# Kernel tuning notes

Hardware: AMD Instinct MI355X
Metric: run time of the kernel (lower is better)

The kernel has to match this reference:

```python
import jax, jax.numpy as jnp
import numpy as np

B, S, DIM = 2, 2048, 2048
NH = 16
Q_LORA, KV_LORA = 1536, 512
NOPE, ROPE, VHD = 128, 64, 128
QK_HD = NOPE + ROPE  # 192
EPS = 1e-6
SCALE = QK_HD ** -0.5


def rmsnorm(x, w, eps=EPS):
    return x * jax.lax.rsqrt(jnp.mean(x * x, axis=-1, keepdims=True) + eps) * w


def apply_rope(x, cos, sin):
    # x: (b, s, h, d) with d even; cos/sin: (s, d//2)
    xr, xi = x[..., 0::2], x[..., 1::2]
    c = cos[None, :, None, :]
    s = sin[None, :, None, :]
    yr = xr * c - xi * s
    yi = xr * s + xi * c
    return jnp.stack([yr, yi], axis=-1).reshape(x.shape)


def setup_inputs() -> dict:
    key = jax.random.key(0)
    ks = jax.random.split(key, 12)
    std = 0.02
    # RoPE tables (unit-magnitude complex as cos/sin)
    inv_freq = 1.0 / (10000.0 ** (np.arange(0, ROPE, 2, dtype=np.float32) / ROPE))  # (32,)
    ang = np.arange(S, dtype=np.float32)[:, None] * inv_freq[None, :]  # (S, 32)
    return {
        "x": jax.random.normal(ks[0], (B, S, DIM), jnp.float32),
        "freqs_cos": jnp.asarray(np.cos(ang)),
        "freqs_sin": jnp.asarray(np.sin(ang)),
        "wq_a_w": jax.random.normal(ks[1], (Q_LORA, DIM), jnp.float32) * std,
        "wq_a_b": jnp.zeros((Q_LORA,), jnp.float32),
        "q_norm_w": jnp.ones((Q_LORA,), jnp.float32),
        "wq_b_w": jax.random.normal(ks[2], (NH * QK_HD, Q_LORA), jnp.float32) * std,
        "wq_b_b": jnp.zeros((NH * QK_HD,), jnp.float32),
        "wkv_a_w": jax.random.normal(ks[3], (KV_LORA + ROPE, DIM), jnp.float32) * std,
        "wkv_a_b": jnp.zeros((KV_LORA + ROPE,), jnp.float32),
        "kv_norm_w": jnp.ones((KV_LORA,), jnp.float32),
        "wkv_b_w": jax.random.normal(ks[4], (NH * (NOPE + VHD), KV_LORA), jnp.float32) * std,
        "wkv_b_b": jnp.zeros((NH * (NOPE + VHD),), jnp.float32),
        "wo_w": jax.random.normal(ks[5], (DIM, NH * VHD), jnp.float32) * std,
        "wo_b": jnp.zeros((DIM,), jnp.float32),
    }


def reference(x, freqs_cos, freqs_sin, wq_a_w, wq_a_b, q_norm_w, wq_b_w, wq_b_b,
              wkv_a_w, wkv_a_b, kv_norm_w, wkv_b_w, wkv_b_b, wo_w, wo_b):
    b, s, _ = x.shape
    # Low-rank Q projection: wq_b(q_norm(wq_a(x)))
    q = rmsnorm(x @ wq_a_w.T + wq_a_b, q_norm_w) @ wq_b_w.T + wq_b_b
    q = q.reshape(b, s, NH, QK_HD)
    q_nope, q_pe = q[..., :NOPE], q[..., NOPE:]
    q = jnp.concatenate([q_nope, apply_rope(q_pe, freqs_cos, freqs_sin)], axis=-1)
    # Low-rank KV projection
    kv = x @ wkv_a_w.T + wkv_a_b  # (b, s, kv_lora + rope)
    kv_c, k_pe = kv[..., :KV_LORA], kv[..., KV_LORA:]
    k_pe = apply_rope(k_pe[:, :, None, :], freqs_cos, freqs_sin)  # (b, s, 1, rope)
    kv = rmsnorm(kv_c, kv_norm_w) @ wkv_b_w.T + wkv_b_b
    kv = kv.reshape(b, s, NH, NOPE + VHD)
    k_nope, v = kv[..., :NOPE], kv[..., NOPE:]
    k = jnp.concatenate([k_nope, jnp.broadcast_to(k_pe, (b, s, NH, ROPE))], axis=-1)
    # Causal SDPA
    scores = jnp.einsum("bqhd,bkhd->bhqk", q, k) * SCALE
    causal = jnp.tril(jnp.ones((s, s), bool))
    scores = jnp.where(causal[None, None], scores, jnp.float32(-1e30))
    attn = jax.nn.softmax(scores, axis=-1)
    out = jnp.einsum("bhqk,bkhd->bqhd", attn, v).reshape(b, s, NH * VHD)
    return out @ wo_w.T + wo_b
```

## Files before the change

kernel.cpp:

```cpp
#include <hip/hip_runtime.h>


typedef __bf16 bf16x8 __attribute__((ext_vector_type(8)));
typedef float f32x4 __attribute__((ext_vector_type(4)));
typedef unsigned short u16;

#define SEQ 2048
#define SCALE 0.07216878364870323f
#define NEGBIG -30000.0f

__device__ __forceinline__ float b2f(u16 u) {
  union { unsigned u; float f; } c; c.u = ((unsigned)u) << 16; return c.f;
}
__device__ __forceinline__ u16 f2b(float f) {
  union { float f; unsigned u; } c; c.f = f;
  unsigned r = (c.u + 0x7fffu + ((c.u >> 16) & 1u)) >> 16;
  return (u16)r;
}
__device__ __forceinline__ uint4 pack8(float4 a, float4 b) {
  union { uint4 v; u16 e[8]; } t;
  t.e[0] = f2b(a.x); t.e[1] = f2b(a.y); t.e[2] = f2b(a.z); t.e[3] = f2b(a.w);
  t.e[4] = f2b(b.x); t.e[5] = f2b(b.y); t.e[6] = f2b(b.z); t.e[7] = f2b(b.w);
  return t.v;
}

#define GLOAD_LDS16(gsrc, ldst)                                              \
  __builtin_amdgcn_global_load_lds(                                          \
      (const __attribute__((address_space(1))) unsigned int*)(gsrc),         \
      (__attribute__((address_space(3))) unsigned int*)(ldst), 16, 0, 0)

__global__ void cvt_kernel(const float* __restrict__ src, u16* __restrict__ dst,
                           long n8) {
  long i = (long)blockIdx.x * 256 + threadIdx.x;
  long stride = (long)gridDim.x * 256;
  for (; i < n8; i += stride) {
    const float4* s = (const float4*)(src + i * 8);
    float4 a = s[0], b = s[1];
    *(uint4*)(dst + i * 8) = pack8(a, b);
  }
}

template <int OF>
__global__ __launch_bounds__(256) void gemm_lds_kernel(
    const u16* __restrict__ X, int lda, const u16* __restrict__ W,
    const float* __restrict__ bias, void* __restrict__ out,
    int N, int K, float oscale) {
  __shared__ alignas(16) u16 As[2][128 * 64];
  __shared__ alignas(16) u16 Bs[2][128 * 64];
  const int tid = threadIdx.x;
  const int wave = tid >> 6, lane = tid & 63;
  const int quad = lane >> 4, l16 = lane & 15;
  const int wr = (wave >> 1) * 64, wc = (wave & 1) * 64;
  const int bm = blockIdx.x * 128, bn = blockIdx.y * 128;
  const int srow0 = wave * 32 + (lane >> 3);
  const int gcol = ((lane & 7) ^ (lane >> 3)) * 8;

  f32x4 acc[4][4] = {};

  auto stage = [&](int buf, int k0) {
#pragma unroll
    for (int p = 0; p < 4; ++p) {
      int row = srow0 + p * 8;
      const u16* ga = X + (size_t)(bm + row) * lda + k0 + gcol;
      const u16* gb = W + (size_t)(bn + row) * K + k0 + gcol;
      char* la = (char*)(&As[buf][0]) + (wave * 4 + p) * 1024;
      char* lb = (char*)(&Bs[buf][0]) + (wave * 4 + p) * 1024;
      GLOAD_LDS16(ga, la);
      GLOAD_LDS16(gb, lb);
    }
  };

  const int nk = K >> 6;
  stage(0, 0);
  int cur = 0;
  for (int kt = 0; kt < nk; ++kt) {
    __syncthreads();
    if (kt + 1 < nk) stage(cur ^ 1, (kt + 1) * 64);
    const u16* as = &As[cur][0];
    const u16* bs = &Bs[cur][0];
#pragma unroll
    for (int kk = 0; kk < 64; kk += 32) {
      const int cs = (kk + quad * 8) ^ ((l16 & 7) * 8);
      bf16x8 a[4], b[4];
#pragma unroll
      for (int i = 0; i < 4; ++i)
        a[i] = *(const bf16x8*)(as + (wr + i * 16 + l16) * 64 + cs);
#pragma unroll
      for (int j = 0; j < 4; ++j)
        b[j] = *(const bf16x8*)(bs + (wc + j * 16 + l16) * 64 + cs);
#pragma unroll
      for (int i = 0; i < 4; ++i)
#pragma unroll
        for (int j = 0; j < 4; ++j)
          acc[i][j] = __builtin_amdgcn_mfma_f32_16x16x32_bf16(a[i], b[j], acc[i][j], 0, 0, 0);
    }
    cur ^= 1;
  }

#pragma unroll
  for (int i = 0; i < 4; ++i)
#pragma unroll
    for (int j = 0; j < 4; ++j) {
      int col = bn + wc + j * 16 + l16;
      float bv = bias[col];
#pragma unroll
      for (int r = 0; r < 4; ++r) {
        int row = bm + wr + i * 16 + quad * 4 + r;
        float v = (acc[i][j][r] + bv) * oscale;
        if (OF) ((float*)out)[(size_t)row * N + col] = v;
        else    ((u16*)out)[(size_t)row * N + col] = f2b(v);
      }
    }
}

template <int XF, int WF, int OF>
__global__ __launch_bounds__(256, 3) void gemm_kernel(
    const void* __restrict__ X, int lda, const void* __restrict__ W,
    const float* __restrict__ bias, void* __restrict__ out,
    int M, int N, int K, float oscale) {
  constexpr int LDT = 72;
  __shared__ alignas(16) u16 As[64 * LDT];
  __shared__ alignas(16) u16 Bs[128 * LDT];
  const int tid = threadIdx.x;
  const int wave = tid >> 6, lane = tid & 63;
  const int quad = lane >> 4, l16 = lane & 15;
  const int bm = blockIdx.x * 64, bn = blockIdx.y * 128;
  const int wn = wave * 32;
  const int srow = tid >> 3;
  const int scol = (tid & 7) * 8;

  f32x4 acc[4][2] = {};

  float4 pa32[2][2], pb32[4][2];
  uint4  pa16[2],    pb16[4];

  auto load_tile = [&](int k0) {
#pragma unroll
    for (int p = 0; p < 2; ++p) {
      size_t off = (size_t)(bm + srow + p * 32) * lda + k0 + scol;
      if (XF) {
        const float* s = (const float*)X + off;
        pa32[p][0] = *(const float4*)s;
        pa32[p][1] = *(const float4*)(s + 4);
      } else {
        pa16[p] = *(const uint4*)((const u16*)X + off);
      }
    }
#pragma unroll
    for (int p = 0; p < 4; ++p) {
      int n = bn + srow + p * 32;
      size_t off = (size_t)n * K + k0 + scol;
      if (WF) {
        if (n < N) {
          const float* s = (const float*)W + off;
          pb32[p][0] = *(const float4*)s;
          pb32[p][1] = *(const float4*)(s + 4);
        } else {
          pb32[p][0] = make_float4(0.f, 0.f, 0.f, 0.f);
          pb32[p][1] = make_float4(0.f, 0.f, 0.f, 0.f);
        }
      } else {
        if (n < N) pb16[p] = *(const uint4*)((const u16*)W + off);
        else { pb16[p].x = pb16[p].y = pb16[p].z = pb16[p].w = 0u; }
      }
    }
  };

  load_tile(0);
  for (int k0 = 0; k0 < K; k0 += 64) {
    __syncthreads();
#pragma unroll
    for (int p = 0; p < 2; ++p) {
      uint4 v;
      if (XF) v = pack8(pa32[p][0], pa32[p][1]); else v = pa16[p];
      *(uint4*)(&As[(srow + p * 32) * LDT + scol]) = v;
    }
#pragma unroll
    for (int p = 0; p < 4; ++p) {
      uint4 v;
      if (WF) v = pack8(pb32[p][0], pb32[p][1]); else v = pb16[p];
      *(uint4*)(&Bs[(srow + p * 32) * LDT + scol]) = v;
    }
    __syncthreads();
    if (k0 + 64 < K) load_tile(k0 + 64);

#pragma unroll
    for (int kk = 0; kk < 64; kk += 32) {
      bf16x8 a[4], b[2];
#pragma unroll
      for (int i = 0; i < 4; ++i)
        a[i] = *(const bf16x8*)(&As[(i * 16 + l16) * LDT + kk + quad * 8]);
#pragma unroll
      for (int j = 0; j < 2; ++j)
        b[j] = *(const bf16x8*)(&Bs[(wn + j * 16 + l16) * LDT + kk + quad * 8]);
#pragma unroll
      for (int i = 0; i < 4; ++i)
#pragma unroll
        for (int j = 0; j < 2; ++j)
          acc[i][j] = __builtin_amdgcn_mfma_f32_16x16x32_bf16(a[i], b[j], acc[i][j], 0, 0, 0);
    }
  }

#pragma unroll
  for (int i = 0; i < 4; ++i)
#pragma unroll
    for (int j = 0; j < 2; ++j) {
      int col = bn + wn + j * 16 + l16;
      if (col < N) {
        float bv = bias[col];
#pragma unroll
        for (int r = 0; r < 4; ++r) {
          int row = bm + i * 16 + quad * 4 + r;
          float v = (acc[i][j][r] + bv) * oscale;
          if (OF) ((float*)out)[(size_t)row * N + col] = v;
          else    ((u16*)out)[(size_t)row * N + col] = f2b(v);
        }
      }
    }
}

__global__ void rmsnorm_kernel(u16* x, const float* __restrict__ w,
                               int C, int stride) {
  size_t base = (size_t)blockIdx.x * stride;
  float s = 0.f;
  for (int c = threadIdx.x; c < C; c += 256) { float v = b2f(x[base + c]); s += v * v; }
#pragma unroll
  for (int off = 32; off > 0; off >>= 1) s += __shfl_xor(s, off, 64);
  __shared__ float red[4];
  if ((threadIdx.x & 63) == 0) red[threadIdx.x >> 6] = s;
  __syncthreads();
  float tot = red[0] + red[1] + red[2] + red[3];
  float scale = rsqrtf(tot / (float)C + 1e-6f);
  for (int c = threadIdx.x; c < C; c += 256)
    x[base + c] = f2b(b2f(x[base + c]) * scale * w[c]);
}

__global__ void rope_kpe_kernel(const u16* __restrict__ kvn,
                                const float* __restrict__ fcos,
                                const float* __restrict__ fsin,
                                u16* __restrict__ kpe) {
  int idx = blockIdx.x * 256 + threadIdx.x;
  int t = idx >> 5, i = idx & 31;
  int s = t & (SEQ - 1);
  float c = fcos[s * 32 + i], sn = fsin[s * 32 + i];
  float xr = b2f(kvn[(size_t)t * 576 + 512 + 2 * i]);
  float xi = b2f(kvn[(size_t)t * 576 + 512 + 2 * i + 1]);
  kpe[(size_t)t * 64 + 2 * i]     = f2b(xr * c - xi * sn);
  kpe[(size_t)t * 64 + 2 * i + 1] = f2b(xr * sn + xi * c);
}

__global__ void rope_q_kernel(u16* q, const float* __restrict__ fcos,
                              const float* __restrict__ fsin) {
  int idx = blockIdx.x * 256 + threadIdx.x;
  int t = idx >> 8, h = (idx >> 5) & 7, i = idx & 31;
  int s = t & (SEQ - 1);
  float c = fcos[s * 32 + i], sn = fsin[s * 32 + i];
  size_t base = (size_t)t * 1536 + h * 192 + 128 + 2 * i;
  float xr = b2f(q[base]), xi = b2f(q[base + 1]);
  q[base]     = f2b(xr * c - xi * sn);
  q[base + 1] = f2b(xr * sn + xi * c);
}

template <int PAIRED>
__global__ __launch_bounds__(256, 2) void attn_kernel(
    const u16* __restrict__ Q0,
    const u16* __restrict__ Q1,
    const u16* __restrict__ KV0,
    const u16* __restrict__ KV1,
    const u16* __restrict__ KPE,
    u16* __restrict__ O,
    int hbase) {
  constexpr int LK = 200;
  constexpr int LP = 72;
  __shared__ alignas(16) u16 Ks[64 * LK];
  __shared__ alignas(16) u16 Ps[64 * LP];
  __shared__ alignas(16) u16 Vs[128 * LP];

  const int tid = threadIdx.x;
  const int wave = tid >> 6, lane = tid & 63;
  const int quad = lane >> 4, l16 = lane & 15;
  const int h = hbase + blockIdx.y;
  const int hl = h & 7;
  const u16* __restrict__ Q   = (h & 8) ? Q1  : Q0;
  const u16* __restrict__ KVB = (h & 8) ? KV1 : KV0;
  const size_t tok0 = (size_t)blockIdx.z * SEQ;

  auto process = [&](int qt) {
    const int q0 = qt * 64;
    bf16x8 qf[6];
    {
      const u16* qp = Q + (tok0 + q0 + wave * 16 + l16) * 1536 + hl * 192 + quad * 8;
#pragma unroll
      for (int c = 0; c < 6; ++c) qf[c] = *(const bf16x8*)(qp + c * 32);
    }

    f32x4 o_acc[8] = {};
    float m_i[4], l_i[4];
#pragma unroll
    for (int r = 0; r < 4; ++r) { m_i[r] = NEGBIG; l_i[r] = 0.f; }

    const int nkt = qt + 1;
    uint4 kreg[6], vreg[4];
    auto load_tile = [&](int kt) {
      int k0 = kt * 64;
#pragma unroll
      for (int p = 0; p < 6; ++p) {
        int flat = tid + p * 256;
        int r = flat / 24, c8 = (flat % 24) * 8;
        const u16* src = (c8 < 128)
            ? (KVB + (tok0 + k0 + r) * 2048 + hl * 256 + c8)
            : (KPE + (tok0 + k0 + r) * 64 + (c8 - 128));
        kreg[p] = *(const uint4*)src;
      }
#pragma unroll
      for (int p = 0; p < 4; ++p) {
        int flat = tid + p * 256;
        int r = flat / 16, c8 = (flat % 16) * 8;
        vreg[p] = *(const uint4*)(KVB + (tok0 + k0 + r) * 2048 + hl * 256 + 128 + c8);
      }
    };

    load_tile(0);
    for (int kt = 0; kt < nkt; ++kt) {
      const int k0 = kt * 64;
      __syncthreads();
#pragma unroll
      for (int p = 0; p < 6; ++p) {
        int flat = tid + p * 256;
        int r = flat / 24, c8 = (flat % 24) * 8;
        *(uint4*)(&Ks[r * LK + c8]) = kreg[p];
      }
#pragma unroll
      for (int p = 0; p < 4; ++p) {
        int flat = tid + p * 256;
        int r = flat / 16, c8 = (flat % 16) * 8;
        union { uint4 v4; u16 e[8]; } t;
        t.v4 = vreg[p];
        int rs = r >> 3, rl = r & 7;
#pragma unroll
        for (int j = 0; j < 8; ++j) {
          int n = c8 + j;
          Vs[n * LP + ((rs ^ ((n >> 3) & 7)) << 3) + rl] = t.e[j];
        }
      }
      __syncthreads();
      if (kt + 1 < nkt) load_tile(kt + 1);

      f32x4 sc[4];
#pragma unroll
      for (int ni = 0; ni < 4; ++ni) {
        f32x4 a = {};
#pragma unroll
        for (int c = 0; c < 6; ++c) {
          bf16x8 kf = *(const bf16x8*)(&Ks[(ni * 16 + l16) * LK + c * 32 + quad * 8]);
          a = __builtin_amdgcn_mfma_f32_16x16x32_bf16(qf[c], kf, a, 0, 0, 0);
        }
        sc[ni] = a;
      }

      const int qrow_base = q0 + wave * 16 + quad * 4;
      if (kt == nkt - 1) {
#pragma unroll
        for (int ni = 0; ni < 4; ++ni) {
          int col = k0 + ni * 16 + l16;
#pragma unroll
          for (int r = 0; r < 4; ++r)
            if (col > qrow_base + r) sc[ni][r] = NEGBIG;
        }
      }

      float mloc[4];
#pragma unroll
      for (int r = 0; r < 4; ++r) mloc[r] = NEGBIG;
#pragma unroll
      for (int ni = 0; ni < 4; ++ni)
#pragma unroll
        for (int r = 0; r < 4; ++r) mloc[r] = fmaxf(mloc[r], sc[ni][r]);
#pragma unroll
      for (int off = 1; off < 16; off <<= 1)
#pragma unroll
        for (int r = 0; r < 4; ++r) mloc[r] = fmaxf(mloc[r], __shfl_xor(mloc[r], off, 64));

      float alpha[4], rsum[4];
#pragma unroll
      for (int r = 0; r < 4; ++r) {
        float mn = fmaxf(m_i[r], mloc[r]);
        alpha[r] = __expf(m_i[r] - mn);
        m_i[r] = mn;
        rsum[r] = 0.f;
      }
#pragma unroll
      for (int ni = 0; ni < 4; ++ni)
#pragma unroll
        for (int r = 0; r < 4; ++r) {
          float p = __expf(sc[ni][r] - m_i[r]);
          sc[ni][r] = p;
          rsum[r] += p;
        }
#pragma unroll
      for (int off = 1; off < 16; off <<= 1)
#pragma unroll
        for (int r = 0; r < 4; ++r) rsum[r] += __shfl_xor(rsum[r], off, 64);
#pragma unroll
      for (int r = 0; r < 4; ++r) l_i[r] = l_i[r] * alpha[r] + rsum[r];

#pragma unroll
      for (int ni = 0; ni < 4; ++ni)
#pragma unroll
        for (int r = 0; r < 4; ++r)
          Ps[(wave * 16 + quad * 4 + r) * LP + ni * 16 + l16] = f2b(sc[ni][r]);

      __syncthreads();

#pragma unroll
      for (int t8 = 0; t8 < 8; ++t8)
#pragma unroll
        for (int r = 0; r < 4; ++r) o_acc[t8][r] *= alpha[r];

      bf16x8 pf0 = *(const bf16x8*)(&Ps[(wave * 16 + l16) * LP + quad * 8]);
      bf16x8 pf1 = *(const bf16x8*)(&Ps[(wave * 16 + l16) * LP + 32 + quad * 8]);
#pragma unroll
      for (int ni = 0; ni < 8; ++ni) {
        int n0 = ni * 16 + l16;
        int sw = (n0 >> 3) & 7;
        bf16x8 vf0 = *(const bf16x8*)(&Vs[n0 * LP + ((quad ^ sw) << 3)]);
        bf16x8 vf1 = *(const bf16x8*)(&Vs[n0 * LP + (((4 + quad) ^ sw) << 3)]);
        o_acc[ni] = __builtin_amdgcn_mfma_f32_16x16x32_bf16(pf0, vf0, o_acc[ni], 0, 0, 0);
        o_acc[ni] = __builtin_amdgcn_mfma_f32_16x16x32_bf16(pf1, vf1, o_acc[ni], 0, 0, 0);
      }
    }

#pragma unroll
    for (int ni = 0; ni < 8; ++ni) {
      int col = h * 128 + ni * 16 + l16;
#pragma unroll
      for (int r = 0; r < 4; ++r) {
        size_t row = tok0 + q0 + wave * 16 + quad * 4 + r;
        O[row * 2048 + col] = f2b(o_acc[ni][r] / l_i[r]);
      }
    }
  };

  if (PAIRED) {
    process(31 - (int)blockIdx.x);
    process((int)blockIdx.x);
  } else {
    process(blockIdx.z == 0 ? (31 - (int)blockIdx.x) : (int)blockIdx.x);
  }
}

extern "C" void kernel_launch(void* const* d_in, const int* in_sizes, int n_in,
                              void* d_out, int out_size, void* d_ws, size_t ws_size,
                              hipStream_t stream) {
  const float* x      = (const float*)d_in[0];
  const float* fcos   = (const float*)d_in[1];
  const float* fsin   = (const float*)d_in[2];
  const float* wqa    = (const float*)d_in[3];
  const float* wqa_b  = (const float*)d_in[4];
  const float* qnw    = (const float*)d_in[5];
  const float* wqb    = (const float*)d_in[6];
  const float* wqb_b  = (const float*)d_in[7];
  const float* wkva   = (const float*)d_in[8];
  const float* wkva_b = (const float*)d_in[9];
  const float* kvnw   = (const float*)d_in[10];
  const float* wkvb   = (const float*)d_in[11];
  const float* wkvb_b = (const float*)d_in[12];
  const float* wo     = (const float*)d_in[13];
  const float* wo_b   = (const float*)d_in[14];

  char* ws = (char*)d_ws;
  u16* qn   = (u16*)(ws + 0);
  u16* kvn  = (u16*)(ws + 12582912);
  u16* kpe  = (u16*)(ws + 17301504);
  u16* qbA  = (u16*)(ws + 17825792);
  u16* kvB  = (u16*)(ws + 30408704);
  u16* ao   = (u16*)(ws + 47185920);

  dim3 blk(256);

  if (ws_size >= 123994112u) {
    u16* xb    = (u16*)(ws + 63963136);
    u16* kvA   = (u16*)(ws + 63963136);
    u16* wqab  = (u16*)(ws + 80740352);
    u16* wkvab = (u16*)(ws + 87031808);
    u16* wqbb  = (u16*)(ws + 89391104);
    u16* wkvbw = (u16*)(ws + 98828288);
    u16* wob   = (u16*)(ws + 103022592);
    u16* qbB   = (u16*)(ws + 111411200);

    cvt_kernel<<<2048, blk, 0, stream>>>(x,    xb,    1048576);
    cvt_kernel<<<1536, blk, 0, stream>>>(wqa,  wqab,   393216);
    cvt_kernel<<< 576, blk, 0, stream>>>(wkva, wkvab,  147456);
    cvt_kernel<<<2048, blk, 0, stream>>>(wqb,  wqbb,   589824);
    cvt_kernel<<<1024, blk, 0, stream>>>(wkvb, wkvbw,  262144);
    cvt_kernel<<<2048, blk, 0, stream>>>(wo,   wob,    524288);

    gemm_lds_kernel<0><<<dim3(32, 12), blk, 0, stream>>>(xb, 2048, wqab, wqa_b, qn, 1536, 2048, 1.0f);
    gemm_kernel<0,0,0><<<dim3(64, 5),  blk, 0, stream>>>(xb, 2048, wkvab, wkva_b, kvn, 4096, 576, 2048, 1.0f);
    rmsnorm_kernel<<<4096, blk, 0, stream>>>(qn, qnw, 1536, 1536);
    rmsnorm_kernel<<<4096, blk, 0, stream>>>(kvn, kvnw, 512, 576);
    rope_kpe_kernel<<<512, blk, 0, stream>>>(kvn, fcos, fsin, kpe);

    gemm_lds_kernel<0><<<dim3(32, 12), blk, 0, stream>>>(qn, 1536, wqbb, wqb_b, qbA, 1536, 1536, SCALE);
    gemm_lds_kernel<0><<<dim3(32, 12), blk, 0, stream>>>(qn, 1536, wqbb + (size_t)1536 * 1536, wqb_b + 1536, qbB, 1536, 1536, SCALE);
    rope_q_kernel<<<4096, blk, 0, stream>>>(qbA, fcos, fsin);
    rope_q_kernel<<<4096, blk, 0, stream>>>(qbB, fcos, fsin);
    gemm_lds_kernel<0><<<dim3(32, 16), blk, 0, stream>>>(kvn, 576, wkvbw, wkvb_b, kvA, 2048, 512, 1.0f);
    gemm_lds_kernel<0><<<dim3(32, 16), blk, 0, stream>>>(kvn, 576, wkvbw + (size_t)2048 * 512, wkvb_b + 2048, kvB, 2048, 512, 1.0f);

    attn_kernel<1><<<dim3(16, 16, 2), blk, 0, stream>>>(qbA, qbB, kvA, kvB, kpe, ao, 0);

    gemm_lds_kernel<1><<<dim3(32, 16), blk, 0, stream>>>(ao, 2048, wob, wo_b, (float*)d_out, 2048, 2048, 1.0f);
  } else if (ws_size >= 111411200u) {
    u16* xb    = (u16*)(ws + 63963136);
    u16* wqab  = (u16*)(ws + 80740352);
    u16* wkvab = (u16*)(ws + 87031808);
    u16* wqbb  = (u16*)(ws + 89391104);
    u16* wkvbw = (u16*)(ws + 98828288);
    u16* wob   = (u16*)(ws + 103022592);

    cvt_kernel<<<2048, blk, 0, stream>>>(x,    xb,    1048576);
    cvt_kernel<<<1536, blk, 0, stream>>>(wqa,  wqab,   393216);
    cvt_kernel<<< 576, blk, 0, stream>>>(wkva, wkvab,  147456);
    cvt_kernel<<<2048, blk, 0, stream>>>(wqb,  wqbb,   589824);
    cvt_kernel<<<1024, blk, 0, stream>>>(wkvb, wkvbw,  262144);
    cvt_kernel<<<2048, blk, 0, stream>>>(wo,   wob,    524288);

    gemm_kernel<0,0,0><<<dim3(64, 12), blk, 0, stream>>>(xb, 2048, wqab, wqa_b, qn, 4096, 1536, 2048, 1.0f);
    gemm_kernel<0,0,0><<<dim3(64, 5),  blk, 0, stream>>>(xb, 2048, wkvab, wkva_b, kvn, 4096, 576, 2048, 1.0f);
    rmsnorm_kernel<<<4096, blk, 0, stream>>>(qn, qnw, 1536, 1536);
    rmsnorm_kernel<<<4096, blk, 0, stream>>>(kvn, kvnw, 512, 576);
    rope_kpe_kernel<<<512, blk, 0, stream>>>(kvn, fcos, fsin, kpe);

    for (int g = 0; g < 2; ++g) {
      const u16* wqb_g   = wqbb + (size_t)g * 1536 * 1536;
      const float* wqb_bg  = wqb_b + g * 1536;
      const u16* wkvb_g  = wkvbw + (size_t)g * 2048 * 512;
      const float* wkvb_bg = wkvb_b + g * 2048;
      gemm_kernel<0,0,0><<<dim3(64, 12), blk, 0, stream>>>(qn, 1536, wqb_g, wqb_bg, qbA, 4096, 1536, 1536, SCALE);
      rope_q_kernel<<<4096, blk, 0, stream>>>(qbA, fcos, fsin);
      gemm_kernel<0,0,0><<<dim3(64, 16), blk, 0, stream>>>(kvn, 576, wkvb_g, wkvb_bg, kvB, 4096, 2048, 512, 1.0f);
      attn_kernel<0><<<dim3(32, 8, 2), blk, 0, stream>>>(qbA, qbA, kvB, kvB, kpe, ao, g * 8);
    }

    gemm_kernel<0,0,1><<<dim3(64, 16), blk, 0, stream>>>(ao, 2048, wob, wo_b, (float*)d_out, 4096, 2048, 2048, 1.0f);
  } else {
    gemm_kernel<1,1,0><<<dim3(64, 12), blk, 0, stream>>>(x, 2048, wqa, wqa_b, qn, 4096, 1536, 2048, 1.0f);
    gemm_kernel<1,1,0><<<dim3(64, 5),  blk, 0, stream>>>(x, 2048, wkva, wkva_b, kvn, 4096, 576, 2048, 1.0f);
    rmsnorm_kernel<<<4096, blk, 0, stream>>>(qn, qnw, 1536, 1536);
    rmsnorm_kernel<<<4096, blk, 0, stream>>>(kvn, kvnw, 512, 576);
    rope_kpe_kernel<<<512, blk, 0, stream>>>(kvn, fcos, fsin, kpe);

    for (int g = 0; g < 2; ++g) {
      const float* wqb_g   = wqb + (size_t)g * 1536 * 1536;
      const float* wqb_bg  = wqb_b + g * 1536;
      const float* wkvb_g  = wkvb + (size_t)g * 2048 * 512;
      const float* wkvb_bg = wkvb_b + g * 2048;
      gemm_kernel<0,1,0><<<dim3(64, 12), blk, 0, stream>>>(qn, 1536, wqb_g, wqb_bg, qbA, 4096, 1536, 1536, SCALE);
      rope_q_kernel<<<4096, blk, 0, stream>>>(qbA, fcos, fsin);
      gemm_kernel<0,1,0><<<dim3(64, 16), blk, 0, stream>>>(kvn, 576, wkvb_g, wkvb_bg, kvB, 4096, 2048, 512, 1.0f);
      attn_kernel<0><<<dim3(32, 8, 2), blk, 0, stream>>>(qbA, qbA, kvB, kvB, kpe, ao, g * 8);
    }

    gemm_kernel<0,1,1><<<dim3(64, 16), blk, 0, stream>>>(ao, 2048, wo, wo_b, (float*)d_out, 4096, 2048, 2048, 1.0f);
  }
}
```

Baseline: 546.1 us.

## Switch LDS GEMMs to 64x128 single-buffered tiles with higher occupancy

Replaces the 128x128 double-buffered global_load_lds GEMM with a 64x128 single-buffered variant, where each wave computes a 64x32 slice. Launch bounds allow 4 blocks per CU. The goal is more blocks and better occupancy and load balance across CUs for these mid-sized GEMMs. It also routes the kv_a projection through this kernel, guarding columns against N=576. In exchange, per-block operand reuse drops and prefetch overlap of the next K tile is lost.

```diff
diff --git a/kernel.cpp b/kernel.cpp
--- a/kernel.cpp
+++ b/kernel.cpp
@@ -41,74 +41,73 @@
 }
 
 template <int OF>
-__global__ __launch_bounds__(256) void gemm_lds_kernel(
+__global__ __launch_bounds__(256, 4) void gemm64_lds_kernel(
     const u16* __restrict__ X, int lda, const u16* __restrict__ W,
     const float* __restrict__ bias, void* __restrict__ out,
     int N, int K, float oscale) {
-  __shared__ alignas(16) u16 As[2][128 * 64];
-  __shared__ alignas(16) u16 Bs[2][128 * 64];
+  __shared__ alignas(16) u16 As[64 * 64];
+  __shared__ alignas(16) u16 Bs[128 * 64];
   const int tid = threadIdx.x;
   const int wave = tid >> 6, lane = tid & 63;
   const int quad = lane >> 4, l16 = lane & 15;
-  const int wr = (wave >> 1) * 64, wc = (wave & 1) * 64;
-  const int bm = blockIdx.x * 128, bn = blockIdx.y * 128;
-  const int srow0 = wave * 32 + (lane >> 3);
+  const int bm = blockIdx.x * 64, bn = blockIdx.y * 128;
+  const int wn = wave * 32;
+  const int srow = wave * 8 + (lane >> 3);
   const int gcol = ((lane & 7) ^ (lane >> 3)) * 8;
 
-  f32x4 acc[4][4] = {};
-
-  auto stage = [&](int buf, int k0) {
+  f32x4 acc[4][2] = {};
+
+  auto stage = [&](int k0) {
+#pragma unroll
+    for (int p = 0; p < 2; ++p) {
+      const u16* ga = X + (size_t)(bm + srow + p * 32) * lda + k0 + gcol;
+      char* la = (char*)As + (p * 4 + wave) * 1024;
+      GLOAD_LDS16(ga, la);
+    }
 #pragma unroll
     for (int p = 0; p < 4; ++p) {
-      int row = srow0 + p * 8;
-      const u16* ga = X + (size_t)(bm + row) * lda + k0 + gcol;
-      const u16* gb = W + (size_t)(bn + row) * K + k0 + gcol;
-      char* la = (char*)(&As[buf][0]) + (wave * 4 + p) * 1024;
-      char* lb = (char*)(&Bs[buf][0]) + (wave * 4 + p) * 1024;
-      GLOAD_LDS16(ga, la);
+      const u16* gb = W + (size_t)(bn + srow + p * 32) * K + k0 + gcol;
+      char* lb = (char*)Bs + (p * 4 + wave) * 1024;
       GLOAD_LDS16(gb, lb);
     }
   };
 
-  const int nk = K >> 6;
-  stage(0, 0);
-  int cur = 0;
-  for (int kt = 0; kt < nk; ++kt) {
+  for (int k0 = 0; k0 < K; k0 += 64) {
+    stage(k0);
     __syncthreads();
-    if (kt + 1 < nk) stage(cur ^ 1, (kt + 1) * 64);
-    const u16* as = &As[cur][0];
-    const u16* bs = &Bs[cur][0];
 #pragma unroll
     for (int kk = 0; kk < 64; kk += 32) {
       const int cs = (kk + quad * 8) ^ ((l16 & 7) * 8);
-      bf16x8 a[4], b[4];
+      bf16x8 a[4], b[2];
 #pragma unroll
       for (int i = 0; i < 4; ++i)
-        a[i] = *(const bf16x8*)(as + (wr + i * 16 + l16) * 64 + cs);
-#pragma unroll
-      for (int j = 0; j < 4; ++j)
-        b[j] = *(const bf16x8*)(bs + (wc + j * 16 + l16) * 64 + cs);
+        a[i] = *(const bf16x8*)(As + (i * 16 + l16) * 64 + cs);
+#pragma unroll
+      for (int j = 0; j < 2; ++j)
+        b[j] = *(const bf16x8*)(Bs + (wn + j * 16 + l16) * 64 + cs);
 #pragma unroll
       for (int i = 0; i < 4; ++i)
 #pragma unroll
-        for (int j = 0; j < 4; ++j)
+        for (int j = 0; j < 2; ++j)
           acc[i][j] = __builtin_amdgcn_mfma_f32_16x16x32_bf16(a[i], b[j], acc[i][j], 0, 0, 0);
     }
-    cur ^= 1;
+    __syncthreads();
   }
 
 #pragma unroll
   for (int i = 0; i < 4; ++i)
 #pragma unroll
-    for (int j = 0; j < 4; ++j) {
-      int col = bn + wc + j * 16 + l16;
-      float bv = bias[col];
-#pragma unroll
-      for (int r = 0; r < 4; ++r) {
-        int row = bm + wr + i * 16 + quad * 4 + r;
-        float v = (acc[i][j][r] + bv) * oscale;
-        if (OF) ((float*)out)[(size_t)row * N + col] = v;
-        else    ((u16*)out)[(size_t)row * N + col] = f2b(v);
+    for (int j = 0; j < 2; ++j) {
+      int col = bn + wn + j * 16 + l16;
+      if (col < N) {
+        float bv = bias[col];
+#pragma unroll
+        for (int r = 0; r < 4; ++r) {
+          int row = bm + i * 16 + quad * 4 + r;
+          float v = (acc[i][j][r] + bv) * oscale;
+          if (OF) ((float*)out)[(size_t)row * N + col] = v;
+          else    ((u16*)out)[(size_t)row * N + col] = f2b(v);
+        }
       }
     }
 }
@@ -495,22 +494,22 @@
     cvt_kernel<<<1024, blk, 0, stream>>>(wkvb, wkvbw,  262144);
     cvt_kernel<<<2048, blk, 0, stream>>>(wo,   wob,    524288);
 
-    gemm_lds_kernel<0><<<dim3(32, 12), blk, 0, stream>>>(xb, 2048, wqab, wqa_b, qn, 1536, 2048, 1.0f);
-    gemm_kernel<0,0,0><<<dim3(64, 5),  blk, 0, stream>>>(xb, 2048, wkvab, wkva_b, kvn, 4096, 576, 2048, 1.0f);
+    gemm64_lds_kernel<0><<<dim3(64, 12), blk, 0, stream>>>(xb, 2048, wqab, wqa_b, qn, 1536, 2048, 1.0f);
+    gemm64_lds_kernel<0><<<dim3(64, 5),  blk, 0, stream>>>(xb, 2048, wkvab, wkva_b, kvn, 576, 2048, 1.0f);
     rmsnorm_kernel<<<4096, blk, 0, stream>>>(qn, qnw, 1536, 1536);
     rmsnorm_kernel<<<4096, blk, 0, stream>>>(kvn, kvnw, 512, 576);
     rope_kpe_kernel<<<512, blk, 0, stream>>>(kvn, fcos, fsin, kpe);
 
-    gemm_lds_kernel<0><<<dim3(32, 12), blk, 0, stream>>>(qn, 1536, wqbb, wqb_b, qbA, 1536, 1536, SCALE);
-    gemm_lds_kernel<0><<<dim3(32, 12), blk, 0, stream>>>(qn, 1536, wqbb + (size_t)1536 * 1536, wqb_b + 1536, qbB, 1536, 1536, SCALE);
+    gemm64_lds_kernel<0><<<dim3(64, 12), blk, 0, stream>>>(qn, 1536, wqbb, wqb_b, qbA, 1536, 1536, SCALE);
+    gemm64_lds_kernel<0><<<dim3(64, 12), blk, 0, stream>>>(qn, 1536, wqbb + (size_t)1536 * 1536, wqb_b + 1536, qbB, 1536, 1536, SCALE);
     rope_q_kernel<<<4096, blk, 0, stream>>>(qbA, fcos, fsin);
     rope_q_kernel<<<4096, blk, 0, stream>>>(qbB, fcos, fsin);
-    gemm_lds_kernel<0><<<dim3(32, 16), blk, 0, stream>>>(kvn, 576, wkvbw, wkvb_b, kvA, 2048, 512, 1.0f);
-    gemm_lds_kernel<0><<<dim3(32, 16), blk, 0, stream>>>(kvn, 576, wkvbw + (size_t)2048 * 512, wkvb_b + 2048, kvB, 2048, 512, 1.0f);
+    gemm64_lds_kernel<0><<<dim3(64, 16), blk, 0, stream>>>(kvn, 576, wkvbw, wkvb_b, kvA, 2048, 512, 1.0f);
+    gemm64_lds_kernel<0><<<dim3(64, 16), blk, 0, stream>>>(kvn, 576, wkvbw + (size_t)2048 * 512, wkvb_b + 2048, kvB, 2048, 512, 1.0f);
 
     attn_kernel<1><<<dim3(16, 16, 2), blk, 0, stream>>>(qbA, qbB, kvA, kvB, kpe, ao, 0);
 
-    gemm_lds_kernel<1><<<dim3(32, 16), blk, 0, stream>>>(ao, 2048, wob, wo_b, (float*)d_out, 2048, 2048, 1.0f);
+    gemm64_lds_kernel<1><<<dim3(64, 16), blk, 0, stream>>>(ao, 2048, wob, wo_b, (float*)d_out, 2048, 2048, 1.0f);
   } else if (ws_size >= 111411200u) {
     u16* xb    = (u16*)(ws + 63963136);
     u16* wqab  = (u16*)(ws + 80740352);
```

New measurement: 556.7 us. No clear change (+1.9%).
